# Optimization experiments

Measured on AMD Instinct MI355X. Metric: run time of the kernel, lower is better.

## Reference

```python
import jax, jax.numpy as jnp
import numpy as np
import math

HIDDEN = 512
N_PROTO = 1024
BATCH = 16384


def setup_inputs() -> dict:
    key = jax.random.key(0)
    kx, kp = jax.random.split(key)
    X = jax.random.normal(kx, (BATCH, HIDDEN), dtype=jnp.float32)
    # prototypes init: uniform in [-k, k], k = 1/sqrt(hidden)
    k = 1.0 / math.sqrt(HIDDEN)
    u = jax.random.uniform(kp, (N_PROTO, HIDDEN), dtype=jnp.float32)
    prototypes = k + (-2.0 * k) * u
    return {"X": X, "prototypes": prototypes}


def reference(X, prototypes):
    # out[b, p] = -sum_h (X[b,h] - prototypes[p,h])^2
    x_sq = jnp.sum(X * X, axis=1, keepdims=True)            # [B, 1]
    p_sq = jnp.sum(prototypes * prototypes, axis=1)[None, :]  # [1, P]
    cross = jnp.einsum("bh,ph->bp", X, prototypes)          # [B, P]
    return -(x_sq + p_sq - 2.0 * cross)
```

## Files before the change

### kernel.cpp

```cpp
#include <hip/hip_runtime.h>
#include <hip/hip_bf16.h>

#define MDIM 16384
#define NDIM 1024
#define KDIM 512
#define BM 256
#define BN 256
#define BK 64
#define KTILES (KDIM / BK)

typedef __attribute__((ext_vector_type(8))) short bf16x8;
typedef __attribute__((ext_vector_type(4))) float f32x4;

__device__ __forceinline__ short f2bf(float f) {
    union { float f; unsigned u; } v; v.f = f;
    unsigned r = v.u + 0x7fff + ((v.u >> 16) & 1);
    return (short)(r >> 16);
}

__device__ __forceinline__ bf16x8 cvt8(float4 a, float4 b) {
    bf16x8 o;
    o[0] = f2bf(a.x); o[1] = f2bf(a.y); o[2] = f2bf(a.z); o[3] = f2bf(a.w);
    o[4] = f2bf(b.x); o[5] = f2bf(b.y); o[6] = f2bf(b.z); o[7] = f2bf(b.w);
    return o;
}

__device__ __forceinline__ void gload_lds16(const void* g, void* l) {
    __builtin_amdgcn_global_load_lds(
        (const __attribute__((address_space(1))) void*)g,
        (__attribute__((address_space(3))) void*)l, 16, 0, 0);
}

__global__ __launch_bounds__(256) void convert_sumsq(
        const float* __restrict__ X, const float* __restrict__ P,
        short* __restrict__ Xbf, short* __restrict__ Pbf,
        float* __restrict__ xsq, float* __restrict__ psq) {
    int wave = (blockIdx.x * blockDim.x + threadIdx.x) >> 6;
    int lane = threadIdx.x & 63;
    const float* src; short* dstb; float* dsts; int row;
    if (wave < MDIM) { src = X; dstb = Xbf; dsts = xsq; row = wave; }
    else             { src = P; dstb = Pbf; dsts = psq; row = wave - MDIM; }
    const float4* r4 = (const float4*)(src + (size_t)row * KDIM) + lane * 2;
    float4 a = r4[0], b = r4[1];
    *(bf16x8*)(dstb + (size_t)row * KDIM + lane * 8) = cvt8(a, b);
    float s = a.x*a.x + a.y*a.y + a.z*a.z + a.w*a.w
            + b.x*b.x + b.y*b.y + b.z*b.z + b.w*b.w;
    #pragma unroll
    for (int off = 32; off; off >>= 1) s += __shfl_down(s, off, 64);
    if (lane == 0) dsts[row] = s;
}

__global__ __launch_bounds__(512, 2) void dist_gemm8(
        const short* __restrict__ Xbf, const short* __restrict__ Pbf,
        const float* __restrict__ xsq, const float* __restrict__ psq,
        float* __restrict__ out) {
    __shared__ short As[2][BM * BK];
    __shared__ short Bs[2][BN * BK];

    int tid = threadIdx.x;
    int bid = blockIdx.x;
    int swz = (bid & 7) * 32 + (bid >> 3);
    int bn = swz & 3, bm = swz >> 2;
    int row0 = bm * BM, col0 = bn * BN;

    int lane = tid & 63, wid = tid >> 6;
    int wr = wid >> 2, wc = wid & 3;

    f32x4 acc[8][4] = {};

    const short* Ab = Xbf + (size_t)row0 * KDIM;
    const short* Bb = Pbf + (size_t)col0 * KDIM;

    auto stageA = [&](int sel, int kt) {
        #pragma unroll
        for (int i = 0; i < 4; ++i) {
            int c = tid + 512 * i;
            int row = c >> 3;
            int g16 = (c & 7) ^ (row & 7);
            const char* ga = (const char*)(Ab + (size_t)row * KDIM)
                             + (size_t)kt * (BK * 2) + g16 * 16;
            gload_lds16(ga, (char*)&As[sel][0] + i * 8192 + wid * 1024);
        }
    };
    auto stageB = [&](int sel, int kt) {
        #pragma unroll
        for (int i = 0; i < 4; ++i) {
            int c = tid + 512 * i;
            int row = c >> 3;
            int g16 = (c & 7) ^ (row & 7);
            const char* gb = (const char*)(Bb + (size_t)row * KDIM)
                             + (size_t)kt * (BK * 2) + g16 * 16;
            gload_lds16(gb, (char*)&Bs[sel][0] + i * 8192 + wid * 1024);
        }
    };

    auto lds_off = [&](int row, int kb) {
        return (row * (BK * 2) + kb) ^ ((row & 7) << 4);
    };

    auto ktile = [&](int sel, int kt) {
        const char* asB = (const char*)&As[sel][0];
        const char* bsB = (const char*)&Bs[sel][0];
        bool more = (kt + 1) < KTILES;
        bf16x8 bfr[4];
        #pragma unroll
        for (int ks = 0; ks < 2; ++ks) {
            int kb = ks * 64 + ((lane >> 4) * 16);
            {
                bf16x8 af[4];
                #pragma unroll
                for (int j = 0; j < 4; ++j)
                    af[j] = *(const bf16x8*)(asB +
                        lds_off(wr * 128 + j * 16 + (lane & 15), kb));
                #pragma unroll
                for (int n = 0; n < 4; ++n)
                    bfr[n] = *(const bf16x8*)(bsB +
                        lds_off(wc * 64 + n * 16 + (lane & 15), kb));
                if (ks == 0 && more) stageA(sel ^ 1, kt + 1);
                __builtin_amdgcn_s_barrier();
                __builtin_amdgcn_s_setprio(1);
                #pragma unroll
                for (int j = 0; j < 4; ++j)
                    #pragma unroll
                    for (int n = 0; n < 4; ++n)
                        acc[j][n] = __builtin_amdgcn_mfma_f32_16x16x32_bf16(
                            af[j], bfr[n], acc[j][n], 0, 0, 0);
                __builtin_amdgcn_s_setprio(0);
                __builtin_amdgcn_s_barrier();
            }
            {
                bf16x8 af[4];
                #pragma unroll
                for (int j = 0; j < 4; ++j)
                    af[j] = *(const bf16x8*)(asB +
                        lds_off(wr * 128 + 64 + j * 16 + (lane & 15), kb));
                if (ks == 0 && more) stageB(sel ^ 1, kt + 1);
                __builtin_amdgcn_s_barrier();
                __builtin_amdgcn_s_setprio(1);
                #pragma unroll
                for (int j = 0; j < 4; ++j)
                    #pragma unroll
                    for (int n = 0; n < 4; ++n)
                        acc[4 + j][n] = __builtin_amdgcn_mfma_f32_16x16x32_bf16(
                            af[j], bfr[n], acc[4 + j][n], 0, 0, 0);
                __builtin_amdgcn_s_setprio(0);
                if (ks == 1) {
                    if (more) asm volatile("s_waitcnt vmcnt(0)" ::: "memory");
                    __builtin_amdgcn_s_barrier();
                    __builtin_amdgcn_sched_barrier(0);
                } else {
                    __builtin_amdgcn_s_barrier();
                }
            }
        }
    };

    stageA(0, 0);
    stageB(0, 0);
    asm volatile("s_waitcnt vmcnt(0)" ::: "memory");
    __builtin_amdgcn_s_barrier();
    __builtin_amdgcn_sched_barrier(0);

    #pragma unroll 1
    for (int p = 0; p < KTILES / 2; ++p) {
        ktile(0, 2 * p);
        ktile(1, 2 * p + 1);
    }

    int cr = (lane >> 4) * 4;
    int cc = lane & 15;
    float ps[4];
    #pragma unroll
    for (int n = 0; n < 4; ++n) ps[n] = psq[col0 + wc * 64 + n * 16 + cc];
    #pragma unroll
    for (int m = 0; m < 8; ++m) {
        int grb = row0 + wr * 128 + m * 16 + cr;
        #pragma unroll
        for (int r = 0; r < 4; ++r) {
            float xv = xsq[grb + r];
            size_t ob = (size_t)(grb + r) * NDIM;
            #pragma unroll
            for (int n = 0; n < 4; ++n) {
                int gc = col0 + wc * 64 + n * 16 + cc;
                out[ob + gc] = 2.0f * acc[m][n][r] - xv - ps[n];
            }
        }
    }
}

__global__ __launch_bounds__(256) void sumsq_kernel(
        const float* __restrict__ X, const float* __restrict__ P,
        float* __restrict__ xsq, float* __restrict__ psq) {
    int wave = (blockIdx.x * blockDim.x + threadIdx.x) >> 6;
    int lane = threadIdx.x & 63;
    const float* src; float* dst; int row;
    if (wave < MDIM) { src = X; dst = xsq; row = wave; }
    else             { src = P; dst = psq; row = wave - MDIM; }
    const float4* r4 = (const float4*)(src + (size_t)row * KDIM) + lane * 2;
    float4 a = r4[0], b = r4[1];
    float s = a.x*a.x + a.y*a.y + a.z*a.z + a.w*a.w
            + b.x*b.x + b.y*b.y + b.z*b.z + b.w*b.w;
    #pragma unroll
    for (int off = 32; off; off >>= 1) s += __shfl_down(s, off, 64);
    if (lane == 0) dst[row] = s;
}

__global__ __launch_bounds__(256) void dist_gemm(
        const float* __restrict__ X, const float* __restrict__ P,
        const float* __restrict__ xsq, const float* __restrict__ psq,
        float* __restrict__ out) {
    __shared__ short As[128 * BK];
    __shared__ short Bs[128 * BK];
    int tid = threadIdx.x;
    int bid = blockIdx.x;
    int swz = (bid & 7) * 128 + (bid >> 3);
    int bn = swz & 7, bm = swz >> 3;
    int row0 = bm * 128, col0 = bn * 128;
    int lane = tid & 63, wid = tid >> 6;
    int wm = (wid >> 1) * 64, wn = (wid & 1) * 64;
    f32x4 acc[4][4] = {};
    int rbase = tid >> 3;
    int kg = tid & 7;
    const float* Abase = X + (size_t)row0 * KDIM;
    const float* Bbase = P + (size_t)col0 * KDIM;
    for (int kt = 0; kt < KDIM / BK; ++kt) {
        int kofs = kt * BK + kg * 8;
        __syncthreads();
        #pragma unroll
        for (int i = 0; i < 4; ++i) {
            int row = rbase + 32 * i;
            const float4* ga = (const float4*)(Abase + (size_t)row * KDIM + kofs);
            float4 a0 = ga[0], a1 = ga[1];
            const float4* gb = (const float4*)(Bbase + (size_t)row * KDIM + kofs);
            float4 b0 = gb[0], b1 = gb[1];
            int off = (row * (BK * 2) + kg * 16) ^ ((row & 7) << 4);
            *(bf16x8*)((char*)As + off) = cvt8(a0, a1);
            *(bf16x8*)((char*)Bs + off) = cvt8(b0, b1);
        }
        __syncthreads();
        #pragma unroll
        for (int ks = 0; ks < 2; ++ks) {
            bf16x8 af[4], bfr[4];
            int kb = ks * 64 + ((lane >> 4) * 16);
            #pragma unroll
            for (int m = 0; m < 4; ++m) {
                int row = wm + m * 16 + (lane & 15);
                int off = (row * (BK * 2) + kb) ^ ((row & 7) << 4);
                af[m] = *(const bf16x8*)((const char*)As + off);
            }
            #pragma unroll
            for (int n = 0; n < 4; ++n) {
                int row = wn + n * 16 + (lane & 15);
                int off = (row * (BK * 2) + kb) ^ ((row & 7) << 4);
                bfr[n] = *(const bf16x8*)((const char*)Bs + off);
            }
            #pragma unroll
            for (int m = 0; m < 4; ++m)
                #pragma unroll
                for (int n = 0; n < 4; ++n)
                    acc[m][n] = __builtin_amdgcn_mfma_f32_16x16x32_bf16(
                        af[m], bfr[n], acc[m][n], 0, 0, 0);
        }
    }
    int cr = (lane >> 4) * 4;
    int cc = lane & 15;
    #pragma unroll
    for (int n = 0; n < 4; ++n) {
        int gc = col0 + wn + n * 16 + cc;
        float ps = psq[gc];
        #pragma unroll
        for (int m = 0; m < 4; ++m) {
            int grb = row0 + wm + m * 16 + cr;
            #pragma unroll
            for (int r = 0; r < 4; ++r) {
                float v = 2.0f * acc[m][n][r] - xsq[grb + r] - ps;
                out[(size_t)(grb + r) * NDIM + gc] = v;
            }
        }
    }
}

extern "C" void kernel_launch(void* const* d_in, const int* in_sizes, int n_in,
                              void* d_out, int out_size, void* d_ws, size_t ws_size,
                              hipStream_t stream) {
    const float* X = (const float*)d_in[0];
    const float* P = (const float*)d_in[1];
    float* out = (float*)d_out;

    const size_t bf_elems = (size_t)(MDIM + NDIM) * KDIM;
    const size_t need = bf_elems * 2 + (size_t)(MDIM + NDIM) * 4;

    if (ws_size >= need) {
        short* Xbf = (short*)d_ws;
        short* Pbf = Xbf + (size_t)MDIM * KDIM;
        float* xsq = (float*)(Xbf + bf_elems);
        float* psq = xsq + MDIM;
        convert_sumsq<<<(MDIM + NDIM) / 4, 256, 0, stream>>>(X, P, Xbf, Pbf, xsq, psq);
        dist_gemm8<<<(MDIM / BM) * (NDIM / BN), 512, 0, stream>>>(Xbf, Pbf, xsq, psq, out);
    } else {
        float* xsq = (float*)d_ws;
        float* psq = xsq + MDIM;
        sumsq_kernel<<<(MDIM + NDIM) / 4, 256, 0, stream>>>(X, P, xsq, psq);
        dist_gemm<<<(MDIM / 128) * (NDIM / 128), 256, 0, stream>>>(X, P, xsq, psq, out);
    }
}
```

Before: 42.14 us.

## Halve the GEMM M tile and switch to a triple-buffered single-barrier pipeline

The distance GEMM now uses 128x256 tiles instead of 256x256, which doubles the grid to 512 blocks. It replaces the double-buffered loop, which had four barriers per k-tile and interleaved staging, with a three-stage LDS ring. Loads run two tiles ahead, gated by vmcnt(6), and there is one barrier per k-tile. The aim is to cut synchronization stalls and hide global-to-LDS latency better. The cost is less register-level reuse of the B tile per block, more total B traffic, and 144KB of LDS per block, which limits residency to one block per CU.

```diff
diff --git a/kernel.cpp b/kernel.cpp
--- a/kernel.cpp
+++ b/kernel.cpp
@@ -4,7 +4,7 @@
 #define MDIM 16384
 #define NDIM 1024
 #define KDIM 512
-#define BM 256
+#define BM 128
 #define BN 256
 #define BK 64
 #define KTILES (KDIM / BK)
@@ -50,47 +50,47 @@
     if (lane == 0) dsts[row] = s;
 }
 
-__global__ __launch_bounds__(512, 2) void dist_gemm8(
+__global__ __launch_bounds__(512, 2) void dist_gemm3s(
         const short* __restrict__ Xbf, const short* __restrict__ Pbf,
         const float* __restrict__ xsq, const float* __restrict__ psq,
         float* __restrict__ out) {
-    __shared__ short As[2][BM * BK];
-    __shared__ short Bs[2][BN * BK];
+    __shared__ short As[3][BM * BK];
+    __shared__ short Bs[3][BN * BK];
 
     int tid = threadIdx.x;
     int bid = blockIdx.x;
-    int swz = (bid & 7) * 32 + (bid >> 3);
+    int swz = (bid & 7) * 64 + (bid >> 3);
     int bn = swz & 3, bm = swz >> 2;
     int row0 = bm * BM, col0 = bn * BN;
 
     int lane = tid & 63, wid = tid >> 6;
     int wr = wid >> 2, wc = wid & 3;
 
-    f32x4 acc[8][4] = {};
+    f32x4 acc[4][4] = {};
 
     const short* Ab = Xbf + (size_t)row0 * KDIM;
     const short* Bb = Pbf + (size_t)col0 * KDIM;
 
     auto stageA = [&](int sel, int kt) {
         #pragma unroll
-        for (int i = 0; i < 4; ++i) {
-            int c = tid + 512 * i;
+        for (int s = 0; s < 2; ++s) {
+            int c = s * 512 + tid;
             int row = c >> 3;
             int g16 = (c & 7) ^ (row & 7);
             const char* ga = (const char*)(Ab + (size_t)row * KDIM)
                              + (size_t)kt * (BK * 2) + g16 * 16;
-            gload_lds16(ga, (char*)&As[sel][0] + i * 8192 + wid * 1024);
+            gload_lds16(ga, (char*)&As[sel][0] + s * 8192 + wid * 1024);
         }
     };
     auto stageB = [&](int sel, int kt) {
         #pragma unroll
-        for (int i = 0; i < 4; ++i) {
-            int c = tid + 512 * i;
+        for (int s = 0; s < 4; ++s) {
+            int c = s * 512 + tid;
             int row = c >> 3;
             int g16 = (c & 7) ^ (row & 7);
             const char* gb = (const char*)(Bb + (size_t)row * KDIM)
                              + (size_t)kt * (BK * 2) + g16 * 16;
-            gload_lds16(gb, (char*)&Bs[sel][0] + i * 8192 + wid * 1024);
+            gload_lds16(gb, (char*)&Bs[sel][0] + s * 8192 + wid * 1024);
         }
     };
 
@@ -98,73 +98,53 @@
         return (row * (BK * 2) + kb) ^ ((row & 7) << 4);
     };
 
-    auto ktile = [&](int sel, int kt) {
-        const char* asB = (const char*)&As[sel][0];
-        const char* bsB = (const char*)&Bs[sel][0];
-        bool more = (kt + 1) < KTILES;
-        bf16x8 bfr[4];
+    auto compute = [&](int sel) {
+        const char* aB = (const char*)&As[sel][0];
+        const char* bB = (const char*)&Bs[sel][0];
         #pragma unroll
         for (int ks = 0; ks < 2; ++ks) {
             int kb = ks * 64 + ((lane >> 4) * 16);
-            {
-                bf16x8 af[4];
-                #pragma unroll
-                for (int j = 0; j < 4; ++j)
-                    af[j] = *(const bf16x8*)(asB +
-                        lds_off(wr * 128 + j * 16 + (lane & 15), kb));
+            bf16x8 af[4], bfr[4];
+            #pragma unroll
+            for (int m = 0; m < 4; ++m)
+                af[m] = *(const bf16x8*)(aB +
+                    lds_off(wr * 64 + m * 16 + (lane & 15), kb));
+            #pragma unroll
+            for (int n = 0; n < 4; ++n)
+                bfr[n] = *(const bf16x8*)(bB +
+                    lds_off(wc * 64 + n * 16 + (lane & 15), kb));
+            __builtin_amdgcn_s_setprio(1);
+            #pragma unroll
+            for (int m = 0; m < 4; ++m)
                 #pragma unroll
                 for (int n = 0; n < 4; ++n)
-                    bfr[n] = *(const bf16x8*)(bsB +
-                        lds_off(wc * 64 + n * 16 + (lane & 15), kb));
-                if (ks == 0 && more) stageA(sel ^ 1, kt + 1);
-                __builtin_amdgcn_s_barrier();
-                __builtin_amdgcn_s_setprio(1);
-                #pragma unroll
-                for (int j = 0; j < 4; ++j)
-                    #pragma unroll
-                    for (int n = 0; n < 4; ++n)
-                        acc[j][n] = __builtin_amdgcn_mfma_f32_16x16x32_bf16(
-                            af[j], bfr[n], acc[j][n], 0, 0, 0);
-                __builtin_amdgcn_s_setprio(0);
-                __builtin_amdgcn_s_barrier();
-            }
-            {
-                bf16x8 af[4];
-                #pragma unroll
-                for (int j = 0; j < 4; ++j)
-                    af[j] = *(const bf16x8*)(asB +
-                        lds_off(wr * 128 + 64 + j * 16 + (lane & 15), kb));
-                if (ks == 0 && more) stageB(sel ^ 1, kt + 1);
-                __builtin_amdgcn_s_barrier();
-                __builtin_amdgcn_s_setprio(1);
-                #pragma unroll
-                for (int j = 0; j < 4; ++j)
-                    #pragma unroll
-                    for (int n = 0; n < 4; ++n)
-                        acc[4 + j][n] = __builtin_amdgcn_mfma_f32_16x16x32_bf16(
-                            af[j], bfr[n], acc[4 + j][n], 0, 0, 0);
-                __builtin_amdgcn_s_setprio(0);
-                if (ks == 1) {
-                    if (more) asm volatile("s_waitcnt vmcnt(0)" ::: "memory");
-                    __builtin_amdgcn_s_barrier();
-                    __builtin_amdgcn_sched_barrier(0);
-                } else {
-                    __builtin_amdgcn_s_barrier();
-                }
-            }
-        }
-    };
-
-    stageA(0, 0);
-    stageB(0, 0);
-    asm volatile("s_waitcnt vmcnt(0)" ::: "memory");
+                    acc[m][n] = __builtin_amdgcn_mfma_f32_16x16x32_bf16(
+                        af[m], bfr[n], acc[m][n], 0, 0, 0);
+            __builtin_amdgcn_s_setprio(0);
+        }
+    };
+
+    stageA(0, 0); stageB(0, 0);
+    stageA(1, 1); stageB(1, 1);
+    asm volatile("s_waitcnt vmcnt(6)" ::: "memory");
     __builtin_amdgcn_s_barrier();
     __builtin_amdgcn_sched_barrier(0);
 
-    #pragma unroll 1
-    for (int p = 0; p < KTILES / 2; ++p) {
-        ktile(0, 2 * p);
-        ktile(1, 2 * p + 1);
+    #pragma unroll
+    for (int t = 0; t < KTILES; ++t) {
+        if (t + 2 < KTILES) {
+            stageA((t + 2) % 3, t + 2);
+            stageB((t + 2) % 3, t + 2);
+        }
+        compute(t % 3);
+        if (t < KTILES - 1) {
+            if (t < KTILES - 2)
+                asm volatile("s_waitcnt vmcnt(6)" ::: "memory");
+            else
+                asm volatile("s_waitcnt vmcnt(0)" ::: "memory");
+            __builtin_amdgcn_s_barrier();
+            __builtin_amdgcn_sched_barrier(0);
+        }
     }
 
     int cr = (lane >> 4) * 4;
@@ -173,8 +153,8 @@
     #pragma unroll
     for (int n = 0; n < 4; ++n) ps[n] = psq[col0 + wc * 64 + n * 16 + cc];
     #pragma unroll
-    for (int m = 0; m < 8; ++m) {
-        int grb = row0 + wr * 128 + m * 16 + cr;
+    for (int m = 0; m < 4; ++m) {
+        int grb = row0 + wr * 64 + m * 16 + cr;
         #pragma unroll
         for (int r = 0; r < 4; ++r) {
             float xv = xsq[grb + r];
@@ -296,7 +276,7 @@
         float* xsq = (float*)(Xbf + bf_elems);
         float* psq = xsq + MDIM;
         convert_sumsq<<<(MDIM + NDIM) / 4, 256, 0, stream>>>(X, P, Xbf, Pbf, xsq, psq);
-        dist_gemm8<<<(MDIM / BM) * (NDIM / BN), 512, 0, stream>>>(Xbf, Pbf, xsq, psq, out);
+        dist_gemm3s<<<(MDIM / BM) * (NDIM / BN), 512, 0, stream>>>(Xbf, Pbf, xsq, psq, out);
     } else {
         float* xsq = (float*)d_ws;
         float* psq = xsq + MDIM;
```

Measured after the change: 42.32 us. About the same (+0.4%).
